# Optimization experiments

Measured on AMD Instinct MI355X. Metric: run time of the kernel, lower is better.

## Reference

```python
import jax, jax.numpy as jnp
import numpy as np
import math

N_HEADS = 8

def setup_inputs() -> dict:
    key = jax.random.key(0)
    qkv = jax.random.normal(key, (4, 1536, 2048), dtype=jnp.float32)
    return {"qkv": qkv}

def reference(qkv) -> jnp.ndarray:
    bs, width, length = qkv.shape
    ch = width // (3 * N_HEADS)
    q, k, v = jnp.split(qkv, 3, axis=1)  # each (bs, n_heads*ch, T)
    scale = 1.0 / math.sqrt(math.sqrt(ch))
    q = (q * scale).reshape(bs * N_HEADS, ch, length)
    k = (k * scale).reshape(bs * N_HEADS, ch, length)
    v = v.reshape(bs * N_HEADS, ch, length)
    # scores: (bs*heads, T, T)
    weight = jnp.einsum('bct,bcs->bts', q, k)
    weight = jax.nn.softmax(weight.astype(jnp.float32), axis=-1).astype(weight.dtype)
    a = jnp.einsum('bts,bcs->bct', weight, v)
    return a.reshape(bs, -1, length)
```

## Files before the change

### kernel.cpp

```cpp
#include <hip/hip_runtime.h>
#include <hip/hip_bf16.h>
#include <math.h>


#define T_LEN 2048
#define NH    32
#define D     64
#define QLD   2048
#define LSTR  72

using f32x4 = __attribute__((ext_vector_type(4))) float;
using s16x8 = __attribute__((ext_vector_type(8))) short;
using s16x4 = __attribute__((ext_vector_type(4))) short;
using u32x4 = __attribute__((ext_vector_type(4))) unsigned;

__device__ __forceinline__ short f2bf(float f) {
    union { float f; unsigned u; } x; x.f = f;
    unsigned r = x.u + 0x7fffu + ((x.u >> 16) & 1u);
    return (short)(r >> 16);
}

#if __has_builtin(__builtin_amdgcn_exp2f)
#define EXP2(x) __builtin_amdgcn_exp2f(x)
#else
#define EXP2(x) __expf(0.6931471805599453f * (x))
#endif

__device__ __forceinline__ unsigned pack2bf(float a, float b) {
    unsigned ua = __float_as_uint(a) + 0x8000u;
    unsigned ub = __float_as_uint(b) + 0x8000u;
    return __builtin_amdgcn_perm(ub, ua, 0x07060302u);
}

__device__ __forceinline__ void cp16(const short* g, short* l) {
    __builtin_amdgcn_global_load_lds(
        (const __attribute__((address_space(1))) void*)g,
        (__attribute__((address_space(3))) void*)l, 16, 0, 0);
}

__global__ __launch_bounds__(256, 4)
void prep(const float* __restrict__ qkv, short* __restrict__ ws16)
{
    __shared__ __align__(16) short tile[64 * LSTR];
    const int tid  = threadIdx.x;
    const int t0   = blockIdx.x * 64;
    const int head = blockIdx.y;
    const int kind = blockIdx.z;
    const int b = head >> 3, h = head & 7;

    short* qt = ws16;
    short* kt = ws16 + (size_t)NH * T_LEN * D;
    short* vb = kt   + (size_t)NH * T_LEN * D;

    if (kind == 2) {
        const float* src = qkv + (size_t)(b * 1536 + 1024 + h * 64) * QLD;
        int c = tid >> 2, seg = (tid & 3) * 16;
        const float* p = src + (size_t)c * QLD + t0 + seg;
        short* dst = vb + ((size_t)head * D + c) * T_LEN + t0 + seg;
        #pragma unroll
        for (int j = 0; j < 2; ++j) {
            f32x4 a  = *(const f32x4*)(p + j * 8);
            f32x4 bb = *(const f32x4*)(p + j * 8 + 4);
            s16x8 w;
            w[0]=f2bf(a[0]);  w[1]=f2bf(a[1]);  w[2]=f2bf(a[2]);  w[3]=f2bf(a[3]);
            w[4]=f2bf(bb[0]); w[5]=f2bf(bb[1]); w[6]=f2bf(bb[2]); w[7]=f2bf(bb[3]);
            *(s16x8*)(dst + j * 8) = w;
        }
        return;
    }

    const float sc = (kind == 0) ? 0.35355339059327373f * 1.4426950408889634f
                                 : 0.35355339059327373f;
    const float* src = qkv + (size_t)(b * 1536 + kind * 512 + h * 64) * QLD;
    short* dst = (kind == 0 ? qt : kt) + ((size_t)head * T_LEN + t0) * D;

    {
        int m = tid & 15, c4 = (tid >> 4) << 2;
        const float* base = src + (size_t)c4 * QLD + t0 + 4 * m;
        f32x4 r0 = *(const f32x4*)base;
        f32x4 r1 = *(const f32x4*)(base + QLD);
        f32x4 r2 = *(const f32x4*)(base + 2 * QLD);
        f32x4 r3 = *(const f32x4*)(base + 3 * QLD);
        #pragma unroll
        for (int j = 0; j < 4; ++j) {
            s16x4 w;
            w[0]=f2bf(r0[j]*sc); w[1]=f2bf(r1[j]*sc); w[2]=f2bf(r2[j]*sc); w[3]=f2bf(r3[j]*sc);
            *(s16x4*)&tile[(4 * m + j) * LSTR + c4] = w;
        }
    }
    __syncthreads();
    {
        int row = tid >> 3;
        int off = (tid & 7) * 8;
        *(s16x8*)(dst + (size_t)row * D + off)        = *(const s16x8*)&tile[row * LSTR + off];
        *(s16x8*)(dst + (size_t)(row + 32) * D + off) = *(const s16x8*)&tile[(row + 32) * LSTR + off];
    }
}

__global__ __launch_bounds__(256, 4)
void attn(const short* __restrict__ ws16, float* __restrict__ out)
{
    __shared__ __align__(16) short ktile[2][64 * 64];
    __shared__ __align__(16) short vtile[2][64 * 64];
    __shared__ float lbuf[4][32];

    const int tid  = threadIdx.x;
    const int w    = tid >> 6;
    const int qh   = w >> 1;
    const int sq   = w & 1;
    const int lane = tid & 63;
    const int l16  = lane & 15;
    const int quad = lane >> 4;

    const int bid  = blockIdx.x;
    const int head = (bid & 7) + 8 * ((bid >> 3) & 3);
    const int t0   = (bid >> 5) * 64;

    const short* qt = ws16 + (size_t)head * T_LEN * D;
    const short* kt = ws16 + (size_t)NH * T_LEN * D + (size_t)head * T_LEN * D;
    const short* vb = ws16 + 2 * (size_t)NH * T_LEN * D + (size_t)head * D * T_LEN;
    float*       op = out  + (size_t)head * 64 * QLD;

    s16x8 bq[2][2];
    #pragma unroll
    for (int nq = 0; nq < 2; ++nq) {
        const short* qrow = qt + (size_t)(t0 + qh * 32 + nq * 16 + l16) * D + quad * 8;
        bq[nq][0] = *(const s16x8*)qrow;
        bq[nq][1] = *(const s16x8*)(qrow + 32);
    }

    s16x8 ones;
    #pragma unroll
    for (int i = 0; i < 8; ++i) ones[i] = (short)0x3F80;

    f32x4 o[2][4];
    f32x4 lacc[2];
    #pragma unroll
    for (int nq = 0; nq < 2; ++nq) {
        lacc[nq] = f32x4{0.f, 0.f, 0.f, 0.f};
        #pragma unroll
        for (int ct = 0; ct < 4; ++ct) o[nq][ct] = f32x4{0.f, 0.f, 0.f, 0.f};
    }

    const int kperm = (l16 >> 2) * 8 + (l16 & 3);
    const int ksw   = (l16 & 3) | (((l16 >> 2) & 1) << 2);
    const int srow  = lane >> 3;
    const int schk  = lane & 7;

    const int rl0 = w * 16 + srow;
    const int rl1 = rl0 + 8;
    const int sk0 = (srow & 3) | (((w * 2 + 0) & 1) << 2);
    const int sk1 = (srow & 3) | (((w * 2 + 1) & 1) << 2);
    const short* kge0 = kt + (size_t)rl0 * D + ((schk ^ sk0) << 3);
    const short* kge1 = kt + (size_t)rl1 * D + ((schk ^ sk1) << 3);
    const short* vge0 = vb + (size_t)rl0 * T_LEN + ((schk ^ srow) << 3);
    const short* vge1 = vb + (size_t)rl1 * T_LEN + ((schk ^ srow) << 3);

    cp16(kge0, &ktile[0][w * 1024]);
    cp16(kge1, &ktile[0][w * 1024 + 512]);
    cp16(vge0, &vtile[0][w * 1024]);
    cp16(vge1, &vtile[0][w * 1024 + 512]);

    const int g = sq;
    #pragma unroll 2
    for (int it = 0; it < T_LEN / 64; ++it) {
        const int cur = it & 1;
        __syncthreads();

        if (it + 1 < T_LEN / 64) {
            const int s0n = (it + 1) * 64;
            cp16(kge0 + (size_t)s0n * D, &ktile[cur ^ 1][w * 1024]);
            cp16(kge1 + (size_t)s0n * D, &ktile[cur ^ 1][w * 1024 + 512]);
            cp16(vge0 + s0n, &vtile[cur ^ 1][w * 1024]);
            cp16(vge1 + s0n, &vtile[cur ^ 1][w * 1024 + 512]);
        }

        u32x4 bp[2];
        #pragma unroll
        for (int sub = 0; sub < 2; ++sub) {
            const int R  = g * 32 + kperm + 4 * sub;
            const int c0 = (quad ^ ksw) << 3;
            s16x8 ak0 = *(const s16x8*)&ktile[cur][R * 64 + c0];
            s16x8 ak1 = *(const s16x8*)&ktile[cur][R * 64 + (c0 ^ 32)];
            #pragma unroll
            for (int nq = 0; nq < 2; ++nq) {
                f32x4 acc = f32x4{0.f, 0.f, 0.f, 0.f};
                acc = __builtin_amdgcn_mfma_f32_16x16x32_bf16(ak0, bq[nq][0], acc, 0, 0, 0);
                acc = __builtin_amdgcn_mfma_f32_16x16x32_bf16(ak1, bq[nq][1], acc, 0, 0, 0);
                bp[nq][sub * 2]     = pack2bf(EXP2(acc[0]), EXP2(acc[1]));
                bp[nq][sub * 2 + 1] = pack2bf(EXP2(acc[2]), EXP2(acc[3]));
            }
        }
        #pragma unroll
        for (int nq = 0; nq < 2; ++nq) {
            lacc[nq] = __builtin_amdgcn_mfma_f32_16x16x32_bf16(
                ones, __builtin_bit_cast(s16x8, bp[nq]), lacc[nq], 0, 0, 0);
            #pragma unroll
            for (int ct = 0; ct < 4; ++ct) {
                const int r = ct * 16 + l16;
                s16x8 av = *(const s16x8*)&vtile[cur][r * 64 + ((((g * 4 + quad) ^ (l16 & 7))) << 3)];
                o[nq][ct] = __builtin_amdgcn_mfma_f32_16x16x32_bf16(
                    av, __builtin_bit_cast(s16x8, bp[nq]), o[nq][ct], 0, 0, 0);
            }
        }
    }

    if (quad == 0) {
        #pragma unroll
        for (int nq = 0; nq < 2; ++nq) lbuf[w][nq * 16 + l16] = lacc[nq][0];
    }
    __syncthreads();

    float* red = (float*)(qh == 0 ? (void*)&ktile[0][0] : (void*)&vtile[0][0]);
    if (sq == 1) {
        #pragma unroll
        for (int nq = 0; nq < 2; ++nq)
            #pragma unroll
            for (int ct = 0; ct < 4; ++ct)
                *(f32x4*)&red[(nq * 16 + l16) * 68 + ct * 16 + quad * 4] = o[nq][ct];
    }
    __syncthreads();
    if (sq == 0) {
        #pragma unroll
        for (int nq = 0; nq < 2; ++nq) {
            const int tr = nq * 16 + l16;
            const float inv = 1.f / (lbuf[qh * 2][tr] + lbuf[qh * 2 + 1][tr]);
            const int tq = t0 + qh * 32 + tr;
            #pragma unroll
            for (int ct = 0; ct < 4; ++ct) {
                f32x4 a = *(const f32x4*)&red[tr * 68 + ct * 16 + quad * 4];
                f32x4 v = o[nq][ct] + a;
                #pragma unroll
                for (int r = 0; r < 4; ++r) {
                    const int c = ct * 16 + quad * 4 + r;
                    op[(size_t)c * QLD + tq] = v[r] * inv;
                }
            }
        }
    }
}

extern "C" void kernel_launch(void* const* d_in, const int* in_sizes, int n_in,
                              void* d_out, int out_size, void* d_ws, size_t ws_size,
                              hipStream_t stream) {
    const float* qkv = (const float*)d_in[0];
    float* out = (float*)d_out;
    short* ws16 = (short*)d_ws;

    prep<<<dim3(T_LEN / 64, NH, 3), dim3(256), 0, stream>>>(qkv, ws16);
    attn<<<dim3(1024), dim3(256), 0, stream>>>(ws16, out);
}
```

Measured before the change: 130.4 us.

## Use hardware bf16 pack, hoist V loads, raise MFMA priority, bump pointers

```diff
diff --git a/kernel.cpp b/kernel.cpp
--- a/kernel.cpp
+++ b/kernel.cpp
@@ -27,9 +27,9 @@
 #endif
 
 __device__ __forceinline__ unsigned pack2bf(float a, float b) {
-    unsigned ua = __float_as_uint(a) + 0x8000u;
-    unsigned ub = __float_as_uint(b) + 0x8000u;
-    return __builtin_amdgcn_perm(ub, ua, 0x07060302u);
+    unsigned r;
+    asm("v_cvt_pk_bf16_f32 %0, %1, %2" : "=v"(r) : "v"(a), "v"(b));
+    return r;
 }
 
 __device__ __forceinline__ void cp16(const short* g, short* l) {
@@ -133,13 +133,15 @@
     #pragma unroll
     for (int i = 0; i < 8; ++i) ones[i] = (short)0x3F80;
 
+    const f32x4 z4 = f32x4{0.f, 0.f, 0.f, 0.f};
+
     f32x4 o[2][4];
     f32x4 lacc[2];
     #pragma unroll
     for (int nq = 0; nq < 2; ++nq) {
-        lacc[nq] = f32x4{0.f, 0.f, 0.f, 0.f};
-        #pragma unroll
-        for (int ct = 0; ct < 4; ++ct) o[nq][ct] = f32x4{0.f, 0.f, 0.f, 0.f};
+        lacc[nq] = z4;
+        #pragma unroll
+        for (int ct = 0; ct < 4; ++ct) o[nq][ct] = z4;
     }
 
     const int kperm = (l16 >> 2) * 8 + (l16 & 3);
@@ -161,6 +163,11 @@
     cp16(vge0, &vtile[0][w * 1024]);
     cp16(vge1, &vtile[0][w * 1024 + 512]);
 
+    const short* kp0 = kge0 + 64 * D;
+    const short* kp1 = kge1 + 64 * D;
+    const short* vp0 = vge0 + 64;
+    const short* vp1 = vge1 + 64;
+
     const int g = sq;
     #pragma unroll 2
     for (int it = 0; it < T_LEN / 64; ++it) {
@@ -168,11 +175,10 @@
         __syncthreads();
 
         if (it + 1 < T_LEN / 64) {
-            const int s0n = (it + 1) * 64;
-            cp16(kge0 + (size_t)s0n * D, &ktile[cur ^ 1][w * 1024]);
-            cp16(kge1 + (size_t)s0n * D, &ktile[cur ^ 1][w * 1024 + 512]);
-            cp16(vge0 + s0n, &vtile[cur ^ 1][w * 1024]);
-            cp16(vge1 + s0n, &vtile[cur ^ 1][w * 1024 + 512]);
+            cp16(kp0, &ktile[cur ^ 1][w * 1024]);        kp0 += 64 * D;
+            cp16(kp1, &ktile[cur ^ 1][w * 1024 + 512]);  kp1 += 64 * D;
+            cp16(vp0, &vtile[cur ^ 1][w * 1024]);        vp0 += 64;
+            cp16(vp1, &vtile[cur ^ 1][w * 1024 + 512]);  vp1 += 64;
         }
 
         u32x4 bp[2];
@@ -184,25 +190,26 @@
             s16x8 ak1 = *(const s16x8*)&ktile[cur][R * 64 + (c0 ^ 32)];
             #pragma unroll
             for (int nq = 0; nq < 2; ++nq) {
-                f32x4 acc = f32x4{0.f, 0.f, 0.f, 0.f};
-                acc = __builtin_amdgcn_mfma_f32_16x16x32_bf16(ak0, bq[nq][0], acc, 0, 0, 0);
+                f32x4 acc;
+                acc = __builtin_amdgcn_mfma_f32_16x16x32_bf16(ak0, bq[nq][0], z4, 0, 0, 0);
                 acc = __builtin_amdgcn_mfma_f32_16x16x32_bf16(ak1, bq[nq][1], acc, 0, 0, 0);
                 bp[nq][sub * 2]     = pack2bf(EXP2(acc[0]), EXP2(acc[1]));
                 bp[nq][sub * 2 + 1] = pack2bf(EXP2(acc[2]), EXP2(acc[3]));
             }
         }
-        #pragma unroll
-        for (int nq = 0; nq < 2; ++nq) {
-            lacc[nq] = __builtin_amdgcn_mfma_f32_16x16x32_bf16(
-                ones, __builtin_bit_cast(s16x8, bp[nq]), lacc[nq], 0, 0, 0);
-            #pragma unroll
-            for (int ct = 0; ct < 4; ++ct) {
-                const int r = ct * 16 + l16;
-                s16x8 av = *(const s16x8*)&vtile[cur][r * 64 + ((((g * 4 + quad) ^ (l16 & 7))) << 3)];
-                o[nq][ct] = __builtin_amdgcn_mfma_f32_16x16x32_bf16(
-                    av, __builtin_bit_cast(s16x8, bp[nq]), o[nq][ct], 0, 0, 0);
-            }
-        }
+        const s16x8 p0 = __builtin_bit_cast(s16x8, bp[0]);
+        const s16x8 p1 = __builtin_bit_cast(s16x8, bp[1]);
+        __builtin_amdgcn_s_setprio(1);
+        lacc[0] = __builtin_amdgcn_mfma_f32_16x16x32_bf16(ones, p0, lacc[0], 0, 0, 0);
+        lacc[1] = __builtin_amdgcn_mfma_f32_16x16x32_bf16(ones, p1, lacc[1], 0, 0, 0);
+        #pragma unroll
+        for (int ct = 0; ct < 4; ++ct) {
+            const int r = ct * 16 + l16;
+            s16x8 av = *(const s16x8*)&vtile[cur][r * 64 + ((((g * 4 + quad) ^ (l16 & 7))) << 3)];
+            o[0][ct] = __builtin_amdgcn_mfma_f32_16x16x32_bf16(av, p0, o[0][ct], 0, 0, 0);
+            o[1][ct] = __builtin_amdgcn_mfma_f32_16x16x32_bf16(av, p1, o[1][ct], 0, 0, 0);
+        }
+        __builtin_amdgcn_s_setprio(0);
     }
 
     if (quad == 0) {
```

After: 127.4 us. -2.3%, faster.
